# Kernel optimization log

Hardware: AMD Instinct MI355X
Metric: run time of the kernel (lower is better)

Reference implementation:

```python
import jax, jax.numpy as jnp
import numpy as np

BLOCK = 256  # query block size for banded computation
NEG = -1e30


def _sliding_window_attention(q, k, v, window_size, block=BLOCK):
    # q, k, v: [B, H, S, D]; mask: |q_idx - kv_idx| <= window_size
    B, H, S, D = q.shape
    w = int(window_size)
    nb = S // block
    Wk = block + 2 * w  # keys visible to one query block
    scale = D ** -0.5

    # pad keys/values by w on each side so every block sees a fixed-size window
    k_pad = jnp.pad(k, ((0, 0), (0, 0), (w, w), (0, 0)))
    v_pad = jnp.pad(v, ((0, 0), (0, 0), (w, w), (0, 0)))

    # padded key indices for each query block: [nb, Wk]
    idx = (jnp.arange(nb) * block)[:, None] + jnp.arange(Wk)[None, :]
    k_win = k_pad[:, :, idx, :]  # [B, H, nb, Wk, D]
    v_win = v_pad[:, :, idx, :]
    qb = q.reshape(B, H, nb, block, D)

    # banded scores: never materialize the full S x S matrix
    scores = jnp.einsum('bhncd,bhnwd->bhncw', qb, k_win) * scale

    a = jnp.arange(block)[:, None]   # query offset within block
    b = jnp.arange(Wk)[None, :]      # key offset within window
    band = (b - a >= 0) & (b - a <= 2 * w)           # |q - kv| <= w
    kv_global = idx - w                               # [nb, Wk]
    valid = (kv_global >= 0) & (kv_global < S)        # exclude padding
    mask = band[None, :, :] & valid[:, None, :]       # [nb, block, Wk]

    scores = jnp.where(mask[None, None], scores, NEG)
    probs = jax.nn.softmax(scores, axis=-1)
    out = jnp.einsum('bhncw,bhnwd->bhncd', probs, v_win)
    return out.reshape(B, H, S, D)


def setup_inputs() -> dict:
    key = jax.random.key(0)
    kq, kk, kv = jax.random.split(key, 3)
    B, H, S, D = 1, 16, 8192, 64
    return {
        'query': jax.random.normal(kq, (B, H, S, D), dtype=jnp.float32),
        'key': jax.random.normal(kk, (B, H, S, D), dtype=jnp.float32),
        'value': jax.random.normal(kv, (B, H, S, D), dtype=jnp.float32),
        'batch_size': 1,
        'window_size': 256,
    }


def reference(query, key, value, batch_size, window_size):
    # batch_size is unused in the original math (signature compatibility only)
    return _sliding_window_attention(query, key, value, window_size)
```

## Files before the change

kernel.cpp:

```cpp
#include <hip/hip_runtime.h>
#include <hip/hip_bf16.h>


#define NH  16
#define SEQ 8192
#define HD  64
#define QT  128
#define NW  8
#define KVB 64
#define NEGV -1e30f
#define NTILE (SEQ / KVB)
#define TILE_ELEMS (KVB * HD)

typedef __bf16 bf16x8 __attribute__((ext_vector_type(8)));
typedef float  f32x4  __attribute__((ext_vector_type(4)));

__device__ __forceinline__ int prow_of(int key) {
    return ((key >> 2) & 1) * 32 + ((key >> 5) & 1) * 16
         + ((key >> 3) & 3) * 4  + (key & 3);
}

__global__ __launch_bounds__(512) void prepack(
    const float* __restrict__ K, const float* __restrict__ V,
    __bf16* __restrict__ kpp, __bf16* __restrict__ vpp)
{
    const int b   = blockIdx.x;
    const int isV = b >= NH * NTILE;
    const int t   = isV ? b - NH * NTILE : b;
    const int tid = threadIdx.x;

    const float* src = (isV ? V : K) + (size_t)t * TILE_ELEMS;
    __bf16*      dst = (isV ? vpp : kpp) + (size_t)t * TILE_ELEMS;

    if (!isV) {
        const int key = tid >> 3, c = tid & 7;
        const float* s = src + key * HD + c * 8;
        float4 a = *(const float4*)s;
        float4 q = *(const float4*)(s + 4);
        bf16x8 o;
        o[0]=(__bf16)a.x; o[1]=(__bf16)a.y; o[2]=(__bf16)a.z; o[3]=(__bf16)a.w;
        o[4]=(__bf16)q.x; o[5]=(__bf16)q.y; o[6]=(__bf16)q.z; o[7]=(__bf16)q.w;
        const int pr = prow_of(key);
        *(bf16x8*)&dst[pr * 64 + ((c * 8) ^ ((pr & 7) << 3))] = o;
    } else {
        __shared__ float Vl[64][65];
        const int key = tid >> 3, c = tid & 7;
        const float* s = src + key * HD + c * 8;
        float4 a = *(const float4*)s;
        float4 q = *(const float4*)(s + 4);
        Vl[key][c*8+0]=a.x; Vl[key][c*8+1]=a.y; Vl[key][c*8+2]=a.z; Vl[key][c*8+3]=a.w;
        Vl[key][c*8+4]=q.x; Vl[key][c*8+5]=q.y; Vl[key][c*8+6]=q.z; Vl[key][c*8+7]=q.w;
        __syncthreads();
        const int vd = tid >> 3, kc = tid & 7;
        bf16x8 o;
#pragma unroll
        for (int j = 0; j < 8; ++j) o[j] = (__bf16)Vl[kc*8 + j][vd];
        *(bf16x8*)&dst[vd * 64 + ((kc * 8) ^ ((vd & 7) << 3))] = o;
    }
}

#define GLOAD_LDS16(G, L)                                                      \
    __builtin_amdgcn_global_load_lds(                                          \
        (const __attribute__((address_space(1))) void*)(G),                    \
        (__attribute__((address_space(3))) void*)(L), 16, 0, 0)

__global__ __launch_bounds__(512) void swa_fwd(
    const float* __restrict__ Q, const __bf16* __restrict__ kpp,
    const __bf16* __restrict__ vpp, float* __restrict__ O,
    const int* __restrict__ wsz)
{
    const int w    = wsz[0];
    const int w2   = 2 * w;

    const int lin = blockIdx.x;
    const int xcd = lin & 7;
    const int i2  = lin >> 3;
    const int h   = 2 * xcd + (i2 >> 6);
    const int q0  = (i2 & 63) * QT;

    const int tid  = threadIdx.x;
    const int lane = tid & 63;
    const int wv   = tid >> 6;
    const int l15  = lane & 15;
    const int g    = lane >> 4;

    const float* Qh = Q + (size_t)h * SEQ * HD;
    float*       Oh = O + (size_t)h * SEQ * HD;

    __shared__ __align__(16) __bf16 Ks[2][TILE_ELEMS];
    __shared__ __align__(16) __bf16 Vt[2][TILE_ELEMS];

    const float qscale = 0.125f * 1.44269504f;
    const int   qrow   = q0 + wv * 16 + l15;
    bf16x8 qf[2];
#pragma unroll
    for (int ks = 0; ks < 2; ++ks) {
        const float* src = Qh + (size_t)qrow * HD + ks*32 + g*8;
        float4 a = *(const float4*)src;
        float4 b = *(const float4*)(src + 4);
        bf16x8 t;
        t[0] = (__bf16)(a.x * qscale); t[1] = (__bf16)(a.y * qscale);
        t[2] = (__bf16)(a.z * qscale); t[3] = (__bf16)(a.w * qscale);
        t[4] = (__bf16)(b.x * qscale); t[5] = (__bf16)(b.y * qscale);
        t[6] = (__bf16)(b.z * qscale); t[7] = (__bf16)(b.w * qscale);
        qf[ks] = t;
    }

    f32x4 acc[4];
    float lrp = 0.f;
#pragma unroll
    for (int db = 0; db < 4; ++db) acc[db] = f32x4{0.f, 0.f, 0.f, 0.f};

    int kv_lo = q0 - w; if (kv_lo < 0) kv_lo = 0; kv_lo &= ~(KVB - 1);
    int kv_hi = q0 + QT + w; if (kv_hi > SEQ) kv_hi = SEQ;
    kv_hi = (kv_hi + KVB - 1) & ~(KVB - 1);
    const int nT = (kv_hi - kv_lo) / KVB;

    const int rw0 = q0 + wv * 16;

    const size_t headTileBase = (size_t)h * NTILE * TILE_ELEMS;
    const int    chunkOff     = wv * 512 + lane * 8;

#define STAGE_TILE(TI, BUF)                                                    \
    {                                                                          \
        const size_t tb = headTileBase + (size_t)(TI) * TILE_ELEMS;            \
        GLOAD_LDS16(kpp + tb + chunkOff, &Ks[BUF][wv * 512]);                  \
        GLOAD_LDS16(vpp + tb + chunkOff, &Vt[BUF][wv * 512]);                  \
    }

#define WG_BARRIER()                                                           \
    asm volatile("s_waitcnt vmcnt(0) lgkmcnt(0)" ::: "memory");                \
    __builtin_amdgcn_sched_barrier(0);                                         \
    __builtin_amdgcn_s_barrier();                                              \
    __builtin_amdgcn_sched_barrier(0);

    STAGE_TILE(kv_lo >> 6, 0);
    WG_BARRIER();

    for (int it = 0; it < nT; ++it) {
        const int kb = kv_lo + it * KVB;
        const __bf16* Kb = &Ks[it & 1][0];
        const __bf16* Vb = &Vt[it & 1][0];

        if (it + 1 < nT) STAGE_TILE((kb >> 6) + 1, (it + 1) & 1);

        if (kb <= rw0 + 15 + w && kb + KVB - 1 >= rw0 - w) {
            const int sw = (l15 & 7) << 3;

            f32x4 st[4];
#pragma unroll
            for (int t = 0; t < 4; ++t) {
                bf16x8 kf0 = *(const bf16x8*)&Kb[(t*16 + l15)*64 + ((     g*8) ^ sw)];
                bf16x8 kf1 = *(const bf16x8*)&Kb[(t*16 + l15)*64 + ((32 + g*8) ^ sw)];
                f32x4 z{0.f, 0.f, 0.f, 0.f};
                z     = __builtin_amdgcn_mfma_f32_16x16x32_bf16(kf0, qf[0], z, 0,0,0);
                st[t] = __builtin_amdgcn_mfma_f32_16x16x32_bf16(kf1, qf[1], z, 0,0,0);
            }

            const bool full = (kb + KVB-1 - rw0 <= w) && (kb - (rw0 + 15) >= -w);
            if (!full) {
                const int relb = kb + g*8 + w - rw0 - l15;
#pragma unroll
                for (int t = 0; t < 4; ++t)
#pragma unroll
                    for (int r = 0; r < 4; ++r)
                        if ((unsigned)(relb + (t&1)*32 + (t>>1)*4 + r) > (unsigned)w2)
                            st[t][r] = NEGV;
            }

            float p[4][4];
#pragma unroll
            for (int t = 0; t < 4; ++t)
#pragma unroll
                for (int r = 0; r < 4; ++r)
                    p[t][r] = __builtin_amdgcn_exp2f(fminf(st[t][r], 80.f));

            float s01 = (p[0][0] + p[0][1]) + (p[0][2] + p[0][3]);
            float s23 = (p[1][0] + p[1][1]) + (p[1][2] + p[1][3]);
            float s45 = (p[2][0] + p[2][1]) + (p[2][2] + p[2][3]);
            float s67 = (p[3][0] + p[3][1]) + (p[3][2] + p[3][3]);
            lrp += (s01 + s23) + (s45 + s67);

#pragma unroll
            for (int kh = 0; kh < 2; ++kh) {
                bf16x8 pf;
                pf[0] = (__bf16)p[kh][0];   pf[1] = (__bf16)p[kh][1];
                pf[2] = (__bf16)p[kh][2];   pf[3] = (__bf16)p[kh][3];
                pf[4] = (__bf16)p[kh+2][0]; pf[5] = (__bf16)p[kh+2][1];
                pf[6] = (__bf16)p[kh+2][2]; pf[7] = (__bf16)p[kh+2][3];
#pragma unroll
                for (int db = 0; db < 4; ++db) {
                    bf16x8 vfr = *(const bf16x8*)&Vb[(db*16 + l15)*64 + ((kh*32 + g*8) ^ sw)];
                    acc[db] = __builtin_amdgcn_mfma_f32_16x16x32_bf16(pf, vfr, acc[db], 0,0,0);
                }
            }
        }

        WG_BARRIER();
    }

    float lr = lrp;
    lr += __shfl_xor(lr, 16);
    lr += __shfl_xor(lr, 32);
    const float il = 1.0f / lr;
    float inv[4];
#pragma unroll
    for (int r = 0; r < 4; ++r) inv[r] = __shfl(il, g*4 + r);
#pragma unroll
    for (int db = 0; db < 4; ++db)
#pragma unroll
        for (int r = 0; r < 4; ++r) {
            const int row = rw0 + g*4 + r;
            Oh[(size_t)row * HD + db*16 + l15] = acc[db][r] * inv[r];
        }
}

__global__ __launch_bounds__(512) void swa_fwd_fb(
    const float* __restrict__ Q, const float* __restrict__ K,
    const float* __restrict__ V, float* __restrict__ O,
    const int* __restrict__ wsz)
{
    const int w    = wsz[0];
    const int w2   = 2 * w;
    const int lin = blockIdx.x;
    const int xcd = lin & 7;
    const int i2  = lin >> 3;
    const int h   = 2 * xcd + (i2 >> 6);
    const int q0  = (i2 & 63) * QT;
    const int tid  = threadIdx.x;
    const int lane = tid & 63;
    const int wv   = tid >> 6;
    const int l15  = lane & 15;
    const int g    = lane >> 4;
    const size_t hoff = (size_t)h * SEQ * HD;
    const float* Qh = Q + hoff;
    const float* Kh = K + hoff;
    const float* Vh = V + hoff;
    float*       Oh = O + hoff;
    __shared__ __align__(16) __bf16 Ks[2][KVB * 64];
    __shared__ __align__(16) __bf16 Vt[2][64 * 64];
    const float qscale = 0.125f * 1.44269504f;
    const int   qrow   = q0 + wv * 16 + l15;
    bf16x8 qf[2];
#pragma unroll
    for (int ks = 0; ks < 2; ++ks) {
        const float* src = Qh + (size_t)qrow * HD + ks*32 + g*8;
        float4 a = *(const float4*)src;
        float4 b = *(const float4*)(src + 4);
        bf16x8 t;
        t[0] = (__bf16)(a.x * qscale); t[1] = (__bf16)(a.y * qscale);
        t[2] = (__bf16)(a.z * qscale); t[3] = (__bf16)(a.w * qscale);
        t[4] = (__bf16)(b.x * qscale); t[5] = (__bf16)(b.y * qscale);
        t[6] = (__bf16)(b.z * qscale); t[7] = (__bf16)(b.w * qscale);
        qf[ks] = t;
    }
    f32x4 acc[4];
    float lrp = 0.f;
#pragma unroll
    for (int db = 0; db < 4; ++db) acc[db] = f32x4{0.f, 0.f, 0.f, 0.f};
    int kv_lo = q0 - w; if (kv_lo < 0) kv_lo = 0; kv_lo &= ~(KVB - 1);
    int kv_hi = q0 + QT + w; if (kv_hi > SEQ) kv_hi = SEQ;
    kv_hi = (kv_hi + KVB - 1) & ~(KVB - 1);
    const int nT = (kv_hi - kv_lo) / KVB;
    const int rw0 = q0 + wv * 16;
    const int kkey = tid >> 3, kd8 = (tid & 7) * 8;
    const int prow = prow_of(kkey);
    const int swk  = (prow & 7) << 3;
    const int vd   = tid & 63, vk0 = (tid >> 6) * 8;
    const int swv  = (vd & 7) << 3;
    float4 kpa, kpb;
    float  vp[8];
#define ISSUE_LOADS_FB(KB)                                                     \
    {                                                                          \
        const float* ksrc = Kh + (size_t)((KB) + kkey) * HD + kd8;             \
        kpa = *(const float4*)ksrc;                                            \
        kpb = *(const float4*)(ksrc + 4);                                      \
        const float* vsrc = Vh + (size_t)((KB) + vk0) * HD + vd;               \
        _Pragma("unroll")                                                      \
        for (int j = 0; j < 8; ++j) vp[j] = vsrc[j * HD];                      \
    }
#define CVT_STORE_FB(BUF)                                                      \
    {                                                                          \
        bf16x8 tk;                                                             \
        tk[0] = (__bf16)kpa.x; tk[1] = (__bf16)kpa.y;                          \
        tk[2] = (__bf16)kpa.z; tk[3] = (__bf16)kpa.w;                          \
        tk[4] = (__bf16)kpb.x; tk[5] = (__bf16)kpb.y;                          \
        tk[6] = (__bf16)kpb.z; tk[7] = (__bf16)kpb.w;                          \
        *(bf16x8*)&Ks[BUF][prow*64 + (kd8 ^ swk)] = tk;                        \
        bf16x8 tv;                                                             \
        _Pragma("unroll")                                                      \
        for (int j = 0; j < 8; ++j) tv[j] = (__bf16)vp[j];                     \
        *(bf16x8*)&Vt[BUF][vd*64 + (vk0 ^ swv)] = tv;                          \
    }
#define WG_BARRIER_FB()                                                        \
    asm volatile("s_waitcnt lgkmcnt(0)" ::: "memory");                         \
    __builtin_amdgcn_sched_barrier(0);                                         \
    __builtin_amdgcn_s_barrier();                                              \
    __builtin_amdgcn_sched_barrier(0);
    ISSUE_LOADS_FB(kv_lo);
    CVT_STORE_FB(0);
    if (nT > 1) ISSUE_LOADS_FB(kv_lo + KVB);
    WG_BARRIER_FB();
    for (int it = 0; it < nT; ++it) {
        const int kb = kv_lo + it * KVB;
        const __bf16* Kb = &Ks[it & 1][0];
        const __bf16* Vb = &Vt[it & 1][0];
        if (kb <= rw0 + 15 + w && kb + KVB - 1 >= rw0 - w) {
            const int sw = (l15 & 7) << 3;
            f32x4 st[4];
#pragma unroll
            for (int t = 0; t < 4; ++t) {
                bf16x8 kf0 = *(const bf16x8*)&Kb[(t*16 + l15)*64 + ((     g*8) ^ sw)];
                bf16x8 kf1 = *(const bf16x8*)&Kb[(t*16 + l15)*64 + ((32 + g*8) ^ sw)];
                f32x4 z{0.f, 0.f, 0.f, 0.f};
                z     = __builtin_amdgcn_mfma_f32_16x16x32_bf16(kf0, qf[0], z, 0,0,0);
                st[t] = __builtin_amdgcn_mfma_f32_16x16x32_bf16(kf1, qf[1], z, 0,0,0);
            }
            const bool full = (kb + KVB-1 - rw0 <= w) && (kb - (rw0 + 15) >= -w);
            if (!full) {
                const int relb = kb + g*8 + w - rw0 - l15;
#pragma unroll
                for (int t = 0; t < 4; ++t)
#pragma unroll
                    for (int r = 0; r < 4; ++r)
                        if ((unsigned)(relb + (t&1)*32 + (t>>1)*4 + r) > (unsigned)w2)
                            st[t][r] = NEGV;
            }
            float p[4][4];
#pragma unroll
            for (int t = 0; t < 4; ++t)
#pragma unroll
                for (int r = 0; r < 4; ++r)
                    p[t][r] = __builtin_amdgcn_exp2f(fminf(st[t][r], 80.f));
            float s01 = (p[0][0] + p[0][1]) + (p[0][2] + p[0][3]);
            float s23 = (p[1][0] + p[1][1]) + (p[1][2] + p[1][3]);
            float s45 = (p[2][0] + p[2][1]) + (p[2][2] + p[2][3]);
            float s67 = (p[3][0] + p[3][1]) + (p[3][2] + p[3][3]);
            lrp += (s01 + s23) + (s45 + s67);
#pragma unroll
            for (int kh = 0; kh < 2; ++kh) {
                bf16x8 pf;
                pf[0] = (__bf16)p[kh][0];   pf[1] = (__bf16)p[kh][1];
                pf[2] = (__bf16)p[kh][2];   pf[3] = (__bf16)p[kh][3];
                pf[4] = (__bf16)p[kh+2][0]; pf[5] = (__bf16)p[kh+2][1];
                pf[6] = (__bf16)p[kh+2][2]; pf[7] = (__bf16)p[kh+2][3];
#pragma unroll
                for (int db = 0; db < 4; ++db) {
                    bf16x8 vfr = *(const bf16x8*)&Vb[(db*16 + l15)*64 + ((kh*32 + g*8) ^ sw)];
                    acc[db] = __builtin_amdgcn_mfma_f32_16x16x32_bf16(pf, vfr, acc[db], 0,0,0);
                }
            }
        }
        if (it + 1 < nT) {
            CVT_STORE_FB((it + 1) & 1);
            if (it + 2 < nT) ISSUE_LOADS_FB(kb + 2 * KVB);
        }
        WG_BARRIER_FB();
    }
    float lr = lrp;
    lr += __shfl_xor(lr, 16);
    lr += __shfl_xor(lr, 32);
    const float il = 1.0f / lr;
    float inv[4];
#pragma unroll
    for (int r = 0; r < 4; ++r) inv[r] = __shfl(il, g*4 + r);
#pragma unroll
    for (int db = 0; db < 4; ++db)
#pragma unroll
        for (int r = 0; r < 4; ++r) {
            const int row = rw0 + g*4 + r;
            Oh[(size_t)row * HD + db*16 + l15] = acc[db][r] * inv[r];
        }
}

extern "C" void kernel_launch(void* const* d_in, const int* in_sizes, int n_in,
                              void* d_out, int out_size, void* d_ws, size_t ws_size,
                              hipStream_t stream) {
    const float* Q   = (const float*)d_in[0];
    const float* K   = (const float*)d_in[1];
    const float* V   = (const float*)d_in[2];
    const int*   wsz = (const int*)d_in[4];
    float* O = (float*)d_out;

    const size_t imgBytes = (size_t)NH * NTILE * TILE_ELEMS * sizeof(__bf16);
    if (ws_size >= 2 * imgBytes) {
        __bf16* kpp = (__bf16*)d_ws;
        __bf16* vpp = (__bf16*)((char*)d_ws + imgBytes);
        prepack<<<dim3(2 * NH * NTILE), dim3(512), 0, stream>>>(K, V, kpp, vpp);
        swa_fwd<<<dim3((SEQ / QT) * NH), dim3(512), 0, stream>>>(Q, kpp, vpp, O, wsz);
    } else {
        swa_fwd_fb<<<dim3((SEQ / QT) * NH), dim3(512), 0, stream>>>(Q, K, V, O, wsz);
    }
}
```

Baseline: 55.97 us.

## Double query tile per workgroup so each wave handles two 16-row blocks

Raises the query tile from 128 to 256 rows. Each wave now computes two 16-row query sub-blocks and reuses every K/V fragment it reads from LDS for both. This halves the number of workgroups and roughly halves the redundant K/V tile loads, since the window overlap between neighbouring query tiles is amortised over more rows. In exchange each wave holds twice the accumulators and scores in registers, and the grid shrinks to 512 blocks, which may lower occupancy and load balance. The fallback kernel is pinned to its old 128-row tiling.

```diff
diff --git a/kernel.cpp b/kernel.cpp
--- a/kernel.cpp
+++ b/kernel.cpp
@@ -5,7 +5,7 @@
 #define NH  16
 #define SEQ 8192
 #define HD  64
-#define QT  128
+#define QT  256
 #define NW  8
 #define KVB 64
 #define NEGV -1e30f
@@ -75,8 +75,8 @@
     const int lin = blockIdx.x;
     const int xcd = lin & 7;
     const int i2  = lin >> 3;
-    const int h   = 2 * xcd + (i2 >> 6);
-    const int q0  = (i2 & 63) * QT;
+    const int h   = 2 * xcd + (i2 >> 5);
+    const int q0  = (i2 & 31) * QT;
 
     const int tid  = threadIdx.x;
     const int lane = tid & 63;
@@ -91,32 +91,36 @@
     __shared__ __align__(16) __bf16 Vt[2][TILE_ELEMS];
 
     const float qscale = 0.125f * 1.44269504f;
-    const int   qrow   = q0 + wv * 16 + l15;
-    bf16x8 qf[2];
-#pragma unroll
-    for (int ks = 0; ks < 2; ++ks) {
-        const float* src = Qh + (size_t)qrow * HD + ks*32 + g*8;
-        float4 a = *(const float4*)src;
-        float4 b = *(const float4*)(src + 4);
-        bf16x8 t;
-        t[0] = (__bf16)(a.x * qscale); t[1] = (__bf16)(a.y * qscale);
-        t[2] = (__bf16)(a.z * qscale); t[3] = (__bf16)(a.w * qscale);
-        t[4] = (__bf16)(b.x * qscale); t[5] = (__bf16)(b.y * qscale);
-        t[6] = (__bf16)(b.z * qscale); t[7] = (__bf16)(b.w * qscale);
-        qf[ks] = t;
-    }
-
-    f32x4 acc[4];
-    float lrp = 0.f;
-#pragma unroll
-    for (int db = 0; db < 4; ++db) acc[db] = f32x4{0.f, 0.f, 0.f, 0.f};
+    bf16x8 qf[2][2];
+#pragma unroll
+    for (int rb = 0; rb < 2; ++rb)
+#pragma unroll
+        for (int ks = 0; ks < 2; ++ks) {
+            const float* src = Qh + (size_t)(q0 + wv*32 + rb*16 + l15) * HD + ks*32 + g*8;
+            float4 a = *(const float4*)src;
+            float4 b = *(const float4*)(src + 4);
+            bf16x8 t;
+            t[0] = (__bf16)(a.x * qscale); t[1] = (__bf16)(a.y * qscale);
+            t[2] = (__bf16)(a.z * qscale); t[3] = (__bf16)(a.w * qscale);
+            t[4] = (__bf16)(b.x * qscale); t[5] = (__bf16)(b.y * qscale);
+            t[6] = (__bf16)(b.z * qscale); t[7] = (__bf16)(b.w * qscale);
+            qf[rb][ks] = t;
+        }
+
+    f32x4 acc[2][4];
+    float lrp[2] = {0.f, 0.f};
+#pragma unroll
+    for (int rb = 0; rb < 2; ++rb)
+#pragma unroll
+        for (int db = 0; db < 4; ++db)
+            acc[rb][db] = f32x4{0.f, 0.f, 0.f, 0.f};
 
     int kv_lo = q0 - w; if (kv_lo < 0) kv_lo = 0; kv_lo &= ~(KVB - 1);
     int kv_hi = q0 + QT + w; if (kv_hi > SEQ) kv_hi = SEQ;
     kv_hi = (kv_hi + KVB - 1) & ~(KVB - 1);
     const int nT = (kv_hi - kv_lo) / KVB;
 
-    const int rw0 = q0 + wv * 16;
+    const int rw0 = q0 + wv * 32;
 
     const size_t headTileBase = (size_t)h * NTILE * TILE_ELEMS;
     const int    chunkOff     = wv * 512 + lane * 8;
@@ -144,54 +148,66 @@
 
         if (it + 1 < nT) STAGE_TILE((kb >> 6) + 1, (it + 1) & 1);
 
-        if (kb <= rw0 + 15 + w && kb + KVB - 1 >= rw0 - w) {
+        if (kb <= rw0 + 31 + w && kb + KVB - 1 >= rw0 - w) {
             const int sw = (l15 & 7) << 3;
 
-            f32x4 st[4];
+            f32x4 st[2][4];
 #pragma unroll
             for (int t = 0; t < 4; ++t) {
                 bf16x8 kf0 = *(const bf16x8*)&Kb[(t*16 + l15)*64 + ((     g*8) ^ sw)];
                 bf16x8 kf1 = *(const bf16x8*)&Kb[(t*16 + l15)*64 + ((32 + g*8) ^ sw)];
-                f32x4 z{0.f, 0.f, 0.f, 0.f};
-                z     = __builtin_amdgcn_mfma_f32_16x16x32_bf16(kf0, qf[0], z, 0,0,0);
-                st[t] = __builtin_amdgcn_mfma_f32_16x16x32_bf16(kf1, qf[1], z, 0,0,0);
-            }
-
-            const bool full = (kb + KVB-1 - rw0 <= w) && (kb - (rw0 + 15) >= -w);
+                f32x4 z0{0.f,0.f,0.f,0.f}, z1{0.f,0.f,0.f,0.f};
+                z0       = __builtin_amdgcn_mfma_f32_16x16x32_bf16(kf0, qf[0][0], z0, 0,0,0);
+                st[0][t] = __builtin_amdgcn_mfma_f32_16x16x32_bf16(kf1, qf[0][1], z0, 0,0,0);
+                z1       = __builtin_amdgcn_mfma_f32_16x16x32_bf16(kf0, qf[1][0], z1, 0,0,0);
+                st[1][t] = __builtin_amdgcn_mfma_f32_16x16x32_bf16(kf1, qf[1][1], z1, 0,0,0);
+            }
+
+            const bool full = (kb + KVB-1 - rw0 <= w) && (kb - (rw0 + 31) >= -w);
             if (!full) {
-                const int relb = kb + g*8 + w - rw0 - l15;
+#pragma unroll
+                for (int rb = 0; rb < 2; ++rb) {
+                    const int relb = kb + g*8 + w - (rw0 + rb*16) - l15;
+#pragma unroll
+                    for (int t = 0; t < 4; ++t)
+#pragma unroll
+                        for (int r = 0; r < 4; ++r)
+                            if ((unsigned)(relb + (t&1)*32 + (t>>1)*4 + r) > (unsigned)w2)
+                                st[rb][t][r] = NEGV;
+                }
+            }
+
+            float p[2][4][4];
+#pragma unroll
+            for (int rb = 0; rb < 2; ++rb) {
 #pragma unroll
                 for (int t = 0; t < 4; ++t)
 #pragma unroll
                     for (int r = 0; r < 4; ++r)
-                        if ((unsigned)(relb + (t&1)*32 + (t>>1)*4 + r) > (unsigned)w2)
-                            st[t][r] = NEGV;
-            }
-
-            float p[4][4];
-#pragma unroll
-            for (int t = 0; t < 4; ++t)
-#pragma unroll
-                for (int r = 0; r < 4; ++r)
-                    p[t][r] = __builtin_amdgcn_exp2f(fminf(st[t][r], 80.f));
-
-            float s01 = (p[0][0] + p[0][1]) + (p[0][2] + p[0][3]);
-            float s23 = (p[1][0] + p[1][1]) + (p[1][2] + p[1][3]);
-            float s45 = (p[2][0] + p[2][1]) + (p[2][2] + p[2][3]);
-            float s67 = (p[3][0] + p[3][1]) + (p[3][2] + p[3][3]);
-            lrp += (s01 + s23) + (s45 + s67);
+                        p[rb][t][r] = __builtin_amdgcn_exp2f(fminf(st[rb][t][r], 80.f));
+                float s01 = (p[rb][0][0] + p[rb][0][1]) + (p[rb][0][2] + p[rb][0][3]);
+                float s23 = (p[rb][1][0] + p[rb][1][1]) + (p[rb][1][2] + p[rb][1][3]);
+                float s45 = (p[rb][2][0] + p[rb][2][1]) + (p[rb][2][2] + p[rb][2][3]);
+                float s67 = (p[rb][3][0] + p[rb][3][1]) + (p[rb][3][2] + p[rb][3][3]);
+                lrp[rb] += (s01 + s23) + (s45 + s67);
+            }
 
 #pragma unroll
             for (int kh = 0; kh < 2; ++kh) {
-                bf16x8 pf;
-                pf[0] = (__bf16)p[kh][0];   pf[1] = (__bf16)p[kh][1];
-                pf[2] = (__bf16)p[kh][2];   pf[3] = (__bf16)p[kh][3];
-                pf[4] = (__bf16)p[kh+2][0]; pf[5] = (__bf16)p[kh+2][1];
-                pf[6] = (__bf16)p[kh+2][2]; pf[7] = (__bf16)p[kh+2][3];
+                bf16x8 pf0, pf1;
+                pf0[0]=(__bf16)p[0][kh][0];   pf0[1]=(__bf16)p[0][kh][1];
+                pf0[2]=(__bf16)p[0][kh][2];   pf0[3]=(__bf16)p[0][kh][3];
+                pf0[4]=(__bf16)p[0][kh+2][0]; pf0[5]=(__bf16)p[0][kh+2][1];
+                pf0[6]=(__bf16)p[0][kh+2][2]; pf0[7]=(__bf16)p[0][kh+2][3];
+                pf1[0]=(__bf16)p[1][kh][0];   pf1[1]=(__bf16)p[1][kh][1];
+                pf1[2]=(__bf16)p[1][kh][2];   pf1[3]=(__bf16)p[1][kh][3];
+                pf1[4]=(__bf16)p[1][kh+2][0]; pf1[5]=(__bf16)p[1][kh+2][1];
+                pf1[6]=(__bf16)p[1][kh+2][2]; pf1[7]=(__bf16)p[1][kh+2][3];
 #pragma unroll
                 for (int db = 0; db < 4; ++db) {
                     bf16x8 vfr = *(const bf16x8*)&Vb[(db*16 + l15)*64 + ((kh*32 + g*8) ^ sw)];
-                    acc[db] = __builtin_amdgcn_mfma_f32_16x16x32_bf16(pf, vfr, acc[db], 0,0,0);
+                    acc[0][db] = __builtin_amdgcn_mfma_f32_16x16x32_bf16(pf0, vfr, acc[0][db], 0,0,0);
+                    acc[1][db] = __builtin_amdgcn_mfma_f32_16x16x32_bf16(pf1, vfr, acc[1][db], 0,0,0);
                 }
             }
         }
@@ -199,20 +215,23 @@
         WG_BARRIER();
     }
 
-    float lr = lrp;
-    lr += __shfl_xor(lr, 16);
-    lr += __shfl_xor(lr, 32);
-    const float il = 1.0f / lr;
-    float inv[4];
-#pragma unroll
-    for (int r = 0; r < 4; ++r) inv[r] = __shfl(il, g*4 + r);
-#pragma unroll
-    for (int db = 0; db < 4; ++db)
-#pragma unroll
-        for (int r = 0; r < 4; ++r) {
-            const int row = rw0 + g*4 + r;
-            Oh[(size_t)row * HD + db*16 + l15] = acc[db][r] * inv[r];
-        }
+#pragma unroll
+    for (int rb = 0; rb < 2; ++rb) {
+        float lr = lrp[rb];
+        lr += __shfl_xor(lr, 16);
+        lr += __shfl_xor(lr, 32);
+        const float il = 1.0f / lr;
+        float inv[4];
+#pragma unroll
+        for (int r = 0; r < 4; ++r) inv[r] = __shfl(il, g*4 + r);
+#pragma unroll
+        for (int db = 0; db < 4; ++db)
+#pragma unroll
+            for (int r = 0; r < 4; ++r) {
+                const int row = rw0 + rb*16 + g*4 + r;
+                Oh[(size_t)row * HD + db*16 + l15] = acc[rb][db][r] * inv[r];
+            }
+    }
 }
 
 __global__ __launch_bounds__(512) void swa_fwd_fb(
@@ -226,7 +245,7 @@
     const int xcd = lin & 7;
     const int i2  = lin >> 3;
     const int h   = 2 * xcd + (i2 >> 6);
-    const int q0  = (i2 & 63) * QT;
+    const int q0  = (i2 & 63) * 128;
     const int tid  = threadIdx.x;
     const int lane = tid & 63;
     const int wv   = tid >> 6;
@@ -259,7 +278,7 @@
 #pragma unroll
     for (int db = 0; db < 4; ++db) acc[db] = f32x4{0.f, 0.f, 0.f, 0.f};
     int kv_lo = q0 - w; if (kv_lo < 0) kv_lo = 0; kv_lo &= ~(KVB - 1);
-    int kv_hi = q0 + QT + w; if (kv_hi > SEQ) kv_hi = SEQ;
+    int kv_hi = q0 + 128 + w; if (kv_hi > SEQ) kv_hi = SEQ;
     kv_hi = (kv_hi + KVB - 1) & ~(KVB - 1);
     const int nT = (kv_hi - kv_lo) / KVB;
     const int rw0 = q0 + wv * 16;
@@ -389,6 +408,6 @@
         prepack<<<dim3(2 * NH * NTILE), dim3(512), 0, stream>>>(K, V, kpp, vpp);
         swa_fwd<<<dim3((SEQ / QT) * NH), dim3(512), 0, stream>>>(Q, kpp, vpp, O, wsz);
     } else {
-        swa_fwd_fb<<<dim3((SEQ / QT) * NH), dim3(512), 0, stream>>>(Q, K, V, O, wsz);
+        swa_fwd_fb<<<dim3((SEQ / 128) * NH), dim3(512), 0, stream>>>(Q, K, V, O, wsz);
     }
 }
```

Measured after the change: 56.65 us. About the same (+1.2%).
